# Optimization experiments

Measured on AMD Instinct MI355X. Metric: run time of the kernel, lower is better.

The kernel has to match this reference:

```python
import jax, jax.numpy as jnp
import numpy as np

B, T, D, H = 2, 2048, 1024, 16
HD = D // H  # 64


def _rotary_tables(t, hd):
    # standard RoPE cos/sin tables, shape [T, hd]
    inv_freq = 1.0 / (10000.0 ** (jnp.arange(0, hd, 2, dtype=jnp.float32) / hd))
    freqs = jnp.arange(t, dtype=jnp.float32)[:, None] * inv_freq[None, :]  # [T, hd/2]
    emb = jnp.concatenate([freqs, freqs], axis=-1)  # [T, hd]
    return jnp.cos(emb), jnp.sin(emb)


def setup_inputs() -> dict:
    key = jax.random.key(0)
    kx, kq, kk, kv, kp = jax.random.split(key, 5)
    x = jax.random.normal(kx, (B, T, D), dtype=jnp.float32)
    cos_t, sin_t = _rotary_tables(T, HD)
    cos = jnp.broadcast_to(cos_t[None], (B, T, HD)).astype(jnp.float32)
    sin = jnp.broadcast_to(sin_t[None], (B, T, HD)).astype(jnp.float32)
    scale = 0.02
    Wq = jax.random.normal(kq, (D, D), dtype=jnp.float32) * scale
    Wk = jax.random.normal(kk, (D, D), dtype=jnp.float32) * scale
    Wv = jax.random.normal(kv, (D, D), dtype=jnp.float32) * scale
    Wp = jax.random.normal(kp, (D, D), dtype=jnp.float32) * scale
    return {"x": x, "cos": cos, "sin": sin, "Wq": Wq, "Wk": Wk, "Wv": Wv, "Wp": Wp}


def _rotate_half(x):
    x1, x2 = jnp.split(x, 2, axis=-1)
    return jnp.concatenate([-x2, x1], axis=-1)


def reference(x, cos, sin, Wq, Wk, Wv, Wp):
    b, t, d = x.shape
    h, hd = H, HD
    # torch Linear: y = x @ W.T
    q = jnp.einsum('btd,ed->bte', x, Wq).reshape(b, t, h, hd)
    k = jnp.einsum('btd,ed->bte', x, Wk).reshape(b, t, h, hd)
    v = jnp.einsum('btd,ed->bte', x, Wv).reshape(b, t, h, hd)
    # RoPE, cos/sin [B,T,hd] -> broadcast over heads (unsqueeze_dim=2)
    c = cos[:, :, None, :]
    s = sin[:, :, None, :]
    q = q * c + _rotate_half(q) * s
    k = k * c + _rotate_half(k) * s
    # causal attention, softmax scale = 1/sqrt(head_dim) (flash_attn default)
    scale = 1.0 / np.sqrt(hd).astype(np.float32)
    scores = jnp.einsum('bqhd,bkhd->bhqk', q, k) * scale  # [B,H,T,T]
    mask = jnp.tril(jnp.ones((t, t), dtype=bool))
    scores = jnp.where(mask[None, None], scores, jnp.finfo(scores.dtype).min)
    probs = jax.nn.softmax(scores, axis=-1)
    out = jnp.einsum('bhqk,bkhd->bqhd', probs, v).reshape(b, t, d)
    return jnp.einsum('btd,ed->bte', out, Wp)
```

## Files before the change

### kernel.cpp

```cpp
#include <hip/hip_runtime.h>
#include <hip/hip_bf16.h>

typedef __attribute__((ext_vector_type(8))) short bf16x8s;
typedef __attribute__((ext_vector_type(4))) float f32x4;
typedef __attribute__((ext_vector_type(16))) float f32x16;
typedef __attribute__((ext_vector_type(4))) __bf16 bf16x4;
typedef __attribute__((ext_vector_type(8))) __bf16 bf16x8;

typedef const __attribute__((address_space(1))) void gvoid_t;
typedef __attribute__((address_space(3))) void lvoid_t;

constexpr int Bc = 2, Tc = 2048, Dc = 1024, Hc = 16, HDc = 64;
constexpr int Mc = Bc * Tc;

__global__ void cvt_all(const float* __restrict__ x,
                        const float* __restrict__ wq, const float* __restrict__ wk,
                        const float* __restrict__ wv, const float* __restrict__ wp,
                        __bf16* __restrict__ xb, __bf16* __restrict__ wb) {
  const int bid = blockIdx.x;
  const float* src;
  __bf16* dst;
  int i;
  if (bid < 4096) {
    src = x; dst = xb; i = (bid * 256 + threadIdx.x) * 4;
  } else {
    const int r = bid - 4096;
    const int w = r >> 10;
    src = (w == 0) ? wq : (w == 1) ? wk : (w == 2) ? wv : wp;
    dst = wb + (size_t)w * (Dc * Dc);
    i = ((r & 1023) * 256 + threadIdx.x) * 4;
  }
  float4 v = *(const float4*)(src + i);
  bf16x4 o;
  o[0] = (__bf16)v.x; o[1] = (__bf16)v.y; o[2] = (__bf16)v.z; o[3] = (__bf16)v.w;
  *(bf16x4*)(dst + i) = o;
}

__launch_bounds__(256, 2)
__global__ void gemm_qkv(const __bf16* __restrict__ A,
                         const __bf16* __restrict__ W,
                         __bf16* __restrict__ outb,
                         __bf16* __restrict__ vtout,
                         const float* __restrict__ cbt,
                         const float* __restrict__ sbt) {
  __shared__ __bf16 smem[2][128 * 64];
  __bf16* Alds = smem[0];
  __bf16* Blds = smem[1];
  const int tid = threadIdx.x;
  const int lane = tid & 63, wid = tid >> 6;
  const int wr = wid >> 1, wc = wid & 1;
  const int lr = lane & 15, lg = lane >> 4;
  const int lid = blockIdx.x + (int)gridDim.x * blockIdx.y;
  const int xcd = lid & 7, g = lid >> 3;
  const int brow = (xcd * 4 + (g & 3)) * 128;
  const int bcol = (g >> 2) * 128;
  const __bf16* Wm = W + (size_t)blockIdx.z * (Dc * Dc);

  f32x4 acc[4][4] = {};

  const char* Ag = (const char*)(A + (size_t)brow * Dc);
  const char* Bg = (const char*)(Wm + (size_t)bcol * Dc);
  const int r0 = tid >> 3;
  const int cb = (tid & 7) * 16;

  for (int k0 = 0; k0 < Dc; k0 += 64) {
#pragma unroll
    for (int i = 0; i < 4; ++i) {
      const int r = i * 32 + r0;
      const int ldsoff = (i * 256 + wid * 64) * 16;
      __builtin_amdgcn_global_load_lds(
          (gvoid_t*)(Ag + (size_t)r * (Dc * 2) + k0 * 2 + cb),
          (lvoid_t*)((char*)Alds + ldsoff), 16, 0, 0);
      __builtin_amdgcn_global_load_lds(
          (gvoid_t*)(Bg + (size_t)r * (Dc * 2) + k0 * 2 + cb),
          (lvoid_t*)((char*)Blds + ldsoff), 16, 0, 0);
    }
    __syncthreads();
#pragma unroll
    for (int kk = 0; kk < 2; ++kk) {
      const int col = kk * 32 + lg * 8;
      bf16x8s af[4], bfv[4];
#pragma unroll
      for (int m = 0; m < 4; ++m)
        af[m] = *(const bf16x8s*)(Alds + (wr * 64 + m * 16 + lr) * 64 + col);
#pragma unroll
      for (int n = 0; n < 4; ++n)
        bfv[n] = *(const bf16x8s*)(Blds + (wc * 64 + n * 16 + lr) * 64 + col);
#pragma unroll
      for (int m = 0; m < 4; ++m)
#pragma unroll
        for (int n = 0; n < 4; ++n)
          acc[m][n] = __builtin_amdgcn_mfma_f32_16x16x32_bf16(af[m], bfv[n], acc[m][n], 0, 0, 0);
    }
    __syncthreads();
  }

  const int z = blockIdx.z;
  if (z == 2) {
    const int bb = brow >> 11, t0b = brow & (Tc - 1);
    __bf16* tile_t = smem[0];
#pragma unroll
    for (int h2 = 0; h2 < 2; ++h2) {
      __syncthreads();
      if (wc == h2) {
#pragma unroll
        for (int n = 0; n < 4; ++n) {
#pragma unroll
          for (int m = 0; m < 4; ++m) {
            bf16x4 pb;
#pragma unroll
            for (int j = 0; j < 4; ++j) pb[j] = (__bf16)acc[m][n][j];
            *(bf16x4*)(tile_t + (n * 16 + lr) * 136 + wr * 64 + m * 16 + lg * 4) = pb;
          }
        }
      }
      __syncthreads();
#pragma unroll
      for (int pass = 0; pass < 4; ++pass) {
        const int r = pass * 16 + (tid >> 4);
        const int c8 = (tid & 15) * 8;
        bf16x8 vvv = *(const bf16x8*)(tile_t + r * 136 + c8);
        const int gn = bcol + h2 * 64 + r;
        const int h = gn >> 6, hd = gn & 63;
        *(bf16x8*)(vtout + (((size_t)bb * Hc + h) * HDc + hd) * Tc + t0b + c8) = vvv;
      }
    }
    return;
  }

  {
    const float scl = (z == 0) ? 0.18033688011112042f : 1.0f;
#pragma unroll
    for (int m = 0; m < 4; ++m) {
#pragma unroll
      for (int j = 0; j < 4; ++j) {
        const int gm = brow + wr * 64 + m * 16 + lg * 4 + j;
        const float* cbase = cbt + (size_t)gm * HDc;
        const float* sbase = sbt + (size_t)gm * HDc;
#pragma unroll
        for (int n = 0; n < 2; ++n) {
          const int i = n * 16 + lr;
          const float c0 = cbase[i], s0 = sbase[i];
          const float v0 = acc[m][n][j], v1 = acc[m][n + 2][j];
          acc[m][n][j]     = (v0 * c0 - v1 * s0) * scl;
          acc[m][n + 2][j] = (v1 * c0 + v0 * s0) * scl;
        }
      }
    }
    __bf16* dst = outb + (size_t)z * ((size_t)Mc * Dc);
#pragma unroll
    for (int m = 0; m < 4; ++m) {
#pragma unroll
      for (int j = 0; j < 4; ++j) {
        const int gm = brow + wr * 64 + m * 16 + lg * 4 + j;
        const int bb = gm >> 11, t = gm & (Tc - 1);
#pragma unroll
        for (int n = 0; n < 4; ++n) {
          const int gn = bcol + wc * 64 + n * 16 + lr;
          const int h = gn >> 6, hd = gn & 63;
          dst[(((size_t)bb * Hc + h) * Tc + t) * HDc + hd] = (__bf16)acc[m][n][j];
        }
      }
    }
  }
}

__launch_bounds__(256, 2)
__global__ void gemm_proj(const __bf16* __restrict__ A, const __bf16* __restrict__ W,
                          float* __restrict__ outf) {
  __shared__ __bf16 Alds[128 * 64];
  __shared__ __bf16 Blds[64 * 64];
  const int tid = threadIdx.x;
  const int lane = tid & 63, wid = tid >> 6;
  const int lr = lane & 15, lg = lane >> 4;
  const int lid = blockIdx.x + (int)gridDim.x * blockIdx.y;
  const int xcd = lid & 7, g = lid >> 3;
  const int brow = (xcd * 4 + (g & 3)) * 128;
  const int bcol = (g >> 2) * 64;
  f32x4 acc[2][4] = {};
  const char* Ag = (const char*)(A + (size_t)brow * Dc);
  const char* Bg = (const char*)(W + (size_t)bcol * Dc);
  const int r0 = tid >> 3;
  const int cb = (tid & 7) * 16;
  for (int k0 = 0; k0 < Dc; k0 += 64) {
#pragma unroll
    for (int i = 0; i < 4; ++i) {
      const int r = i * 32 + r0;
      const int ldsoff = (i * 256 + wid * 64) * 16;
      __builtin_amdgcn_global_load_lds(
          (gvoid_t*)(Ag + (size_t)r * (Dc * 2) + k0 * 2 + cb),
          (lvoid_t*)((char*)Alds + ldsoff), 16, 0, 0);
    }
#pragma unroll
    for (int i = 0; i < 2; ++i) {
      const int r = i * 32 + r0;
      const int ldsoff = (i * 256 + wid * 64) * 16;
      __builtin_amdgcn_global_load_lds(
          (gvoid_t*)(Bg + (size_t)r * (Dc * 2) + k0 * 2 + cb),
          (lvoid_t*)((char*)Blds + ldsoff), 16, 0, 0);
    }
    __syncthreads();
#pragma unroll
    for (int kk = 0; kk < 2; ++kk) {
      const int col = kk * 32 + lg * 8;
      bf16x8s af[2], bfv[4];
#pragma unroll
      for (int m = 0; m < 2; ++m)
        af[m] = *(const bf16x8s*)(Alds + (wid * 32 + m * 16 + lr) * 64 + col);
#pragma unroll
      for (int n = 0; n < 4; ++n)
        bfv[n] = *(const bf16x8s*)(Blds + (n * 16 + lr) * 64 + col);
#pragma unroll
      for (int m = 0; m < 2; ++m)
#pragma unroll
        for (int n = 0; n < 4; ++n)
          acc[m][n] = __builtin_amdgcn_mfma_f32_16x16x32_bf16(bfv[n], af[m], acc[m][n], 0, 0, 0);
    }
    __syncthreads();
  }
#pragma unroll
  for (int m = 0; m < 2; ++m) {
    const int gm = brow + wid * 32 + m * 16 + lr;
    float* rowp = outf + (size_t)gm * Dc + bcol;
#pragma unroll
    for (int n = 0; n < 4; ++n) {
      float4 fv;
      fv.x = acc[m][n][0]; fv.y = acc[m][n][1]; fv.z = acc[m][n][2]; fv.w = acc[m][n][3];
      *(float4*)(rowp + n * 16 + lg * 4) = fv;
    }
  }
}

__launch_bounds__(512, 4)
__global__ void attn_kernel(const __bf16* __restrict__ Q, const __bf16* __restrict__ K,
                            const __bf16* __restrict__ Vt, __bf16* __restrict__ O) {
  __shared__ __bf16 Klds[2][128 * 64];
  __shared__ __bf16 Vlds[2][64 * 128];
  const int f = blockIdx.x;
  const int xcd = f & 7, g = f >> 3;
  const int pass = g >> 4, g4 = g & 15;
  const int bh = xcd * 4 + pass;
  const int qt = ((pass >> 1) & 1) ? (15 - g4) : g4;
  const int tid = threadIdx.x;
  const int lane = tid & 63, wid = tid >> 6;
  const int qq = wid >> 1, kp = wid & 1;
  const int q31 = lane & 31, hh = lane >> 5;
  const int k3 = q31 & 7;
  const int v15 = q31 & 15;
  const __bf16* Qp = Q + (size_t)bh * Tc * HDc;
  const char* Kb = (const char*)(K + (size_t)bh * Tc * HDc);
  const char* Vb = (const char*)(Vt + (size_t)bh * HDc * Tc);

  const int units = qt + 1;

  const int sr = tid >> 3;
  const int sxor = ((tid & 7) ^ (sr & 7)) << 4;
  const int vr = tid >> 4;
  const int vxor = ((tid & 15) ^ (vr & 15)) << 4;
  const char* vsrc = Vb + (size_t)vr * (Tc * 2) + vxor;

  const int q0w = qt * 128 + qq * 32;
  bf16x8s qf[4];
#pragma unroll
  for (int ks = 0; ks < 4; ++ks)
    qf[ks] = *(const bf16x8s*)(Qp + (q0w + q31) * HDc + ks * 16 + hh * 8);

  const int b = bh >> 4, h = bh & 15;

  f32x16 acc0 = {}, acc1 = {};
  float lsum = 0.f;

#define STAGE(IT, BUF)                                                                   \
  do {                                                                                   \
    _Pragma("unroll")                                                                    \
    for (int i_ = 0; i_ < 2; ++i_) {                                                     \
      __builtin_amdgcn_global_load_lds(                                                  \
          (gvoid_t*)(Kb + (size_t)((IT) * 128 + i_ * 64 + sr) * 128 + sxor),             \
          (lvoid_t*)((char*)Klds[BUF] + i_ * 8192 + wid * 1024), 16, 0, 0);              \
      __builtin_amdgcn_global_load_lds(                                                  \
          (gvoid_t*)(vsrc + (size_t)i_ * 32 * (Tc * 2) + (IT) * 256),                    \
          (lvoid_t*)((char*)Vlds[BUF] + i_ * 8192 + wid * 1024), 16, 0, 0);              \
    }                                                                                    \
  } while (0)

  STAGE(0, 0);
  asm volatile("s_waitcnt vmcnt(0)" ::: "memory");
  __builtin_amdgcn_sched_barrier(0);
  __builtin_amdgcn_s_barrier();
  __builtin_amdgcn_sched_barrier(0);

  for (int u = 0; u < units; ++u) {
    if (u + 1 < units) STAGE(u + 1, (u + 1) & 1);
    __builtin_amdgcn_sched_barrier(0);

    const bool last = (u == qt);
    if (!(last && kp == 1 && qq < 2)) {
      const char* Kl = (const char*)Klds[u & 1];
      const char* Vl = (const char*)Vlds[u & 1];
      const bool fin = last && ((qq >> 1) == kp);
      const int thr = q0w + q31 - u * 128 - kp * 64 - 4 * hh;

#pragma unroll
      for (int ct = 0; ct < 2; ++ct) {
        bf16x8s kf[4];
#pragma unroll
        for (int ks = 0; ks < 4; ++ks)
          kf[ks] = *(const bf16x8s*)(Kl + (kp * 64 + ct * 32 + q31) * 128 +
                                     (((2 * ks + hh) ^ k3) << 4));
        f32x16 z = {};
        __builtin_amdgcn_s_setprio(1);
#pragma unroll
        for (int ks = 0; ks < 4; ++ks)
          z = __builtin_amdgcn_mfma_f32_32x32x16_bf16(kf[ks], qf[ks], z, 0, 0, 0);
        __builtin_amdgcn_s_setprio(0);

        unsigned w0[4], w1[4];
#pragma unroll
        for (int n = 0; n < 4; ++n) {
          float e[4];
#pragma unroll
          for (int j = 0; j < 4; ++j) {
            float ev = __builtin_amdgcn_exp2f(z[n * 4 + j]);
            if (fin && (ct * 32 + n * 8 + j > thr)) ev = 0.f;
            lsum += ev;
            e[j] = ev;
          }
          asm("v_cvt_pk_bf16_f32 %0, %1, %2" : "=v"(w0[n]) : "v"(e[0]), "v"(e[1]));
          asm("v_cvt_pk_bf16_f32 %0, %1, %2" : "=v"(w1[n]) : "v"(e[2]), "v"(e[3]));
        }

        bf16x8s pfr[2];
#pragma unroll
        for (int ks2 = 0; ks2 < 2; ++ks2) {
          unsigned a = w0[2 * ks2], bb2 = w0[2 * ks2 + 1];
          unsigned c = w1[2 * ks2], d = w1[2 * ks2 + 1];
          asm volatile("v_permlane32_swap_b32 %0, %1" : "+v"(a), "+v"(bb2));
          asm volatile("v_permlane32_swap_b32 %0, %1" : "+v"(c), "+v"(d));
          union { unsigned u[4]; bf16x8s v; } uu;
          uu.u[0] = a; uu.u[1] = c; uu.u[2] = bb2; uu.u[3] = d;
          pfr[ks2] = uu.v;
        }

        __builtin_amdgcn_s_setprio(1);
#pragma unroll
        for (int ks2 = 0; ks2 < 2; ++ks2) {
          const int so = ((kp * 8 + ct * 4 + 2 * ks2 + hh) ^ v15) << 4;
          const bf16x8s va0 = *(const bf16x8s*)(Vl + q31 * 256 + so);
          const bf16x8s va1 = *(const bf16x8s*)(Vl + (32 + q31) * 256 + so);
          acc0 = __builtin_amdgcn_mfma_f32_32x32x16_bf16(va0, pfr[ks2], acc0, 0, 0, 0);
          acc1 = __builtin_amdgcn_mfma_f32_32x32x16_bf16(va1, pfr[ks2], acc1, 0, 0, 0);
        }
        __builtin_amdgcn_s_setprio(0);
      }
    }

    if (u + 1 < units) {
      asm volatile("s_waitcnt vmcnt(0)" ::: "memory");
      __builtin_amdgcn_sched_barrier(0);
      __builtin_amdgcn_s_barrier();
      __builtin_amdgcn_sched_barrier(0);
    }
  }
#undef STAGE

  __syncthreads();
  float* kscr = (float*)&Klds[0][0];
  float* lscr = (float*)&Vlds[0][0];
  if (kp == 1) {
#pragma unroll
    for (int i = 0; i < 16; ++i) {
      kscr[qq * 2048 + i * 64 + lane] = acc0[i];
      kscr[qq * 2048 + 1024 + i * 64 + lane] = acc1[i];
    }
    lscr[qq * 64 + lane] = lsum;
  }
  __syncthreads();
  if (kp == 0) {
#pragma unroll
    for (int i = 0; i < 16; ++i) {
      acc0[i] += kscr[qq * 2048 + i * 64 + lane];
      acc1[i] += kscr[qq * 2048 + 1024 + i * 64 + lane];
    }
    lsum += lscr[qq * 64 + lane];
    const float lt = lsum + __shfl_xor(lsum, 32);
    const float linv = 1.f / lt;
    const int t = q0w + q31;
    __bf16* dst = O + ((size_t)b * Tc + t) * Dc + h * HDc;
#pragma unroll
    for (int qd = 0; qd < 4; ++qd) {
      bf16x4 o0, o1;
#pragma unroll
      for (int j = 0; j < 4; ++j) {
        o0[j] = (__bf16)(acc0[qd * 4 + j] * linv);
        o1[j] = (__bf16)(acc1[qd * 4 + j] * linv);
      }
      *(bf16x4*)(dst + qd * 8 + hh * 4) = o0;
      *(bf16x4*)(dst + 32 + qd * 8 + hh * 4) = o1;
    }
  }
}

extern "C" void kernel_launch(void* const* d_in, const int* in_sizes, int n_in,
                              void* d_out, int out_size, void* d_ws, size_t ws_size,
                              hipStream_t stream) {
  const float* x   = (const float*)d_in[0];
  const float* cbt = (const float*)d_in[1];
  const float* sbt = (const float*)d_in[2];
  const float* Wq  = (const float*)d_in[3];
  const float* Wk  = (const float*)d_in[4];
  const float* Wv  = (const float*)d_in[5];
  const float* Wp  = (const float*)d_in[6];
  float* out = (float*)d_out;
  char* ws = (char*)d_ws;
  __bf16* xb = (__bf16*)(ws);
  __bf16* wb = (__bf16*)(ws + (8u << 20));
  __bf16* qb = (__bf16*)(ws + (16u << 20));
  __bf16* vt = (__bf16*)(ws + (40u << 20));
  __bf16* ao = (__bf16*)(ws + (48u << 20));
  __bf16* kb = qb + (size_t)Mc * Dc;

  cvt_all<<<8192, 256, 0, stream>>>(x, Wq, Wk, Wv, Wp, xb, wb);
  gemm_qkv<<<dim3(8, 32, 3), 256, 0, stream>>>(xb, wb, qb, vt, cbt, sbt);
  attn_kernel<<<512, 512, 0, stream>>>(qb, kb, vt, ao);
  gemm_proj<<<dim3(16, 32), 256, 0, stream>>>(ao, wb + 3u * (Dc * Dc), out);
}
```

Measured before the change: 95.30 us.

## Fuse Q/K/V GEMMs into one block with double-buffered swizzled LDS

The QKV projection kernel now computes the Q, K and V output tiles for the same 128-row A tile in a single 512-thread block. Each A tile is staged once instead of three times. Global-to-LDS loads are double-buffered so the next K-slice is fetched while MFMAs run on the current one. LDS columns are XOR-swizzled to reduce bank conflicts, and MFMA sections raise wave priority. The cost is a large LDS footprint of about 128KB, which limits the kernel to one block per CU. The grid also shrinks to 256 blocks, which removes the z-dimension parallelism.

```diff
diff --git a/kernel.cpp b/kernel.cpp
--- a/kernel.cpp
+++ b/kernel.cpp
@@ -36,130 +36,142 @@
   *(bf16x4*)(dst + i) = o;
 }
 
-__launch_bounds__(256, 2)
+__launch_bounds__(512, 2)
 __global__ void gemm_qkv(const __bf16* __restrict__ A,
                          const __bf16* __restrict__ W,
                          __bf16* __restrict__ outb,
                          __bf16* __restrict__ vtout,
                          const float* __restrict__ cbt,
                          const float* __restrict__ sbt) {
-  __shared__ __bf16 smem[2][128 * 64];
-  __bf16* Alds = smem[0];
-  __bf16* Blds = smem[1];
+  __shared__ __bf16 Albuf[2][128 * 64];
+  __shared__ __bf16 Bbuf[2][3][128 * 64];
   const int tid = threadIdx.x;
   const int lane = tid & 63, wid = tid >> 6;
   const int wr = wid >> 1, wc = wid & 1;
   const int lr = lane & 15, lg = lane >> 4;
-  const int lid = blockIdx.x + (int)gridDim.x * blockIdx.y;
+  const int lid = blockIdx.x + 8 * blockIdx.y;
   const int xcd = lid & 7, g = lid >> 3;
   const int brow = (xcd * 4 + (g & 3)) * 128;
   const int bcol = (g >> 2) * 128;
-  const __bf16* Wm = W + (size_t)blockIdx.z * (Dc * Dc);
-
-  f32x4 acc[4][4] = {};
+
+  f32x4 acc[3][2][4] = {};
 
   const char* Ag = (const char*)(A + (size_t)brow * Dc);
-  const char* Bg = (const char*)(Wm + (size_t)bcol * Dc);
-  const int r0 = tid >> 3;
-  const int cb = (tid & 7) * 16;
-
-  for (int k0 = 0; k0 < Dc; k0 += 64) {
-#pragma unroll
-    for (int i = 0; i < 4; ++i) {
-      const int r = i * 32 + r0;
-      const int ldsoff = (i * 256 + wid * 64) * 16;
-      __builtin_amdgcn_global_load_lds(
-          (gvoid_t*)(Ag + (size_t)r * (Dc * 2) + k0 * 2 + cb),
-          (lvoid_t*)((char*)Alds + ldsoff), 16, 0, 0);
-      __builtin_amdgcn_global_load_lds(
-          (gvoid_t*)(Bg + (size_t)r * (Dc * 2) + k0 * 2 + cb),
-          (lvoid_t*)((char*)Blds + ldsoff), 16, 0, 0);
-    }
-    __syncthreads();
+  const char* Bg = (const char*)(W + (size_t)bcol * Dc);
+  const int r0s = tid >> 3;
+  const int scol = (((tid & 7) ^ (r0s & 7)) << 4);
+  const int lr7 = lr & 7;
+
+#define STAGE(K0, BUF)                                                                    \
+  do {                                                                                    \
+    _Pragma("unroll")                                                                     \
+    for (int i_ = 0; i_ < 2; ++i_) {                                                      \
+      __builtin_amdgcn_global_load_lds(                                                   \
+          (gvoid_t*)(Ag + (size_t)(i_ * 64 + r0s) * (Dc * 2) + (K0)*2 + scol),            \
+          (lvoid_t*)((char*)Albuf[BUF] + i_ * 8192 + wid * 1024), 16, 0, 0);              \
+      _Pragma("unroll")                                                                   \
+      for (int z_ = 0; z_ < 3; ++z_)                                                      \
+        __builtin_amdgcn_global_load_lds(                                                 \
+            (gvoid_t*)(Bg + (size_t)z_ * (Dc * Dc * 2) +                                  \
+                       (size_t)(i_ * 64 + r0s) * (Dc * 2) + (K0)*2 + scol),               \
+            (lvoid_t*)((char*)Bbuf[BUF][z_] + i_ * 8192 + wid * 1024), 16, 0, 0);         \
+    }                                                                                     \
+  } while (0)
+
+  STAGE(0, 0);
+  asm volatile("s_waitcnt vmcnt(0)" ::: "memory");
+  __builtin_amdgcn_sched_barrier(0);
+  __builtin_amdgcn_s_barrier();
+  __builtin_amdgcn_sched_barrier(0);
+
+  for (int s = 0; s < 16; ++s) {
+    if (s + 1 < 16) STAGE((s + 1) * 64, (s + 1) & 1);
+    __builtin_amdgcn_sched_barrier(0);
+    const char* Al = (const char*)Albuf[s & 1];
+    const char* Bl0 = (const char*)Bbuf[s & 1][0];
 #pragma unroll
     for (int kk = 0; kk < 2; ++kk) {
-      const int col = kk * 32 + lg * 8;
-      bf16x8s af[4], bfv[4];
-#pragma unroll
-      for (int m = 0; m < 4; ++m)
-        af[m] = *(const bf16x8s*)(Alds + (wr * 64 + m * 16 + lr) * 64 + col);
-#pragma unroll
-      for (int n = 0; n < 4; ++n)
-        bfv[n] = *(const bf16x8s*)(Blds + (wc * 64 + n * 16 + lr) * 64 + col);
-#pragma unroll
-      for (int m = 0; m < 4; ++m)
+      const int sw = ((kk * 4 + lg) ^ lr7) << 4;
+      bf16x8s af[2];
+#pragma unroll
+      for (int m = 0; m < 2; ++m)
+        af[m] = *(const bf16x8s*)(Al + (wr * 32 + m * 16 + lr) * 128 + sw);
+#pragma unroll
+      for (int z = 0; z < 3; ++z) {
+        const char* Bl = Bl0 + z * (128 * 64 * 2);
+        bf16x8s bfv[4];
 #pragma unroll
         for (int n = 0; n < 4; ++n)
-          acc[m][n] = __builtin_amdgcn_mfma_f32_16x16x32_bf16(af[m], bfv[n], acc[m][n], 0, 0, 0);
-    }
-    __syncthreads();
-  }
-
-  const int z = blockIdx.z;
-  if (z == 2) {
-    const int bb = brow >> 11, t0b = brow & (Tc - 1);
-    __bf16* tile_t = smem[0];
+          bfv[n] = *(const bf16x8s*)(Bl + (wc * 64 + n * 16 + lr) * 128 + sw);
+        __builtin_amdgcn_s_setprio(1);
+#pragma unroll
+        for (int m = 0; m < 2; ++m)
+#pragma unroll
+          for (int n = 0; n < 4; ++n)
+            acc[z][m][n] =
+                __builtin_amdgcn_mfma_f32_16x16x32_bf16(af[m], bfv[n], acc[z][m][n], 0, 0, 0);
+        __builtin_amdgcn_s_setprio(0);
+      }
+    }
+    asm volatile("s_waitcnt vmcnt(0)" ::: "memory");
+    __builtin_amdgcn_sched_barrier(0);
+    __builtin_amdgcn_s_barrier();
+    __builtin_amdgcn_sched_barrier(0);
+  }
+#undef STAGE
+
+  const int h = (bcol >> 6) + wc;
+#pragma unroll
+  for (int z = 0; z < 2; ++z) {
+    const float scl = (z == 0) ? 0.18033688011112042f : 1.0f;
+    __bf16* dst = outb + (size_t)z * ((size_t)Mc * Dc);
+#pragma unroll
+    for (int m = 0; m < 2; ++m) {
+#pragma unroll
+      for (int j = 0; j < 4; ++j) {
+        const int gm = brow + wr * 32 + m * 16 + lg * 4 + j;
+        const int bb = gm >> 11, t = gm & (Tc - 1);
+        const float* cbase = cbt + (size_t)gm * HDc;
+        const float* sbase = sbt + (size_t)gm * HDc;
+#pragma unroll
+        for (int n = 0; n < 2; ++n) {
+          const int i = n * 16 + lr;
+          const float c0 = cbase[i], s0 = sbase[i];
+          const float v0 = acc[z][m][n][j], v1 = acc[z][m][n + 2][j];
+          acc[z][m][n][j]     = (v0 * c0 - v1 * s0) * scl;
+          acc[z][m][n + 2][j] = (v1 * c0 + v0 * s0) * scl;
+        }
+        __bf16* rowp = dst + (((size_t)bb * Hc + h) * Tc + t) * HDc;
+#pragma unroll
+        for (int n = 0; n < 4; ++n) rowp[n * 16 + lr] = (__bf16)acc[z][m][n][j];
+      }
+    }
+  }
+
+  {
+    const int bb2 = brow >> 11, t0b = brow & (Tc - 1);
+    __bf16* tile_t = (__bf16*)Albuf;
 #pragma unroll
     for (int h2 = 0; h2 < 2; ++h2) {
       __syncthreads();
       if (wc == h2) {
 #pragma unroll
-        for (int n = 0; n < 4; ++n) {
-#pragma unroll
-          for (int m = 0; m < 4; ++m) {
-            bf16x4 pb;
-#pragma unroll
-            for (int j = 0; j < 4; ++j) pb[j] = (__bf16)acc[m][n][j];
-            *(bf16x4*)(tile_t + (n * 16 + lr) * 136 + wr * 64 + m * 16 + lg * 4) = pb;
-          }
-        }
+        for (int n = 0; n < 4; ++n)
+#pragma unroll
+          for (int m = 0; m < 2; ++m)
+#pragma unroll
+            for (int j = 0; j < 4; ++j)
+              tile_t[(n * 16 + lr) * 136 + wr * 32 + m * 16 + lg * 4 + j] =
+                  (__bf16)acc[2][m][n][j];
       }
       __syncthreads();
-#pragma unroll
-      for (int pass = 0; pass < 4; ++pass) {
-        const int r = pass * 16 + (tid >> 4);
+      const int hh2 = (bcol >> 6) + h2;
+#pragma unroll
+      for (int p = 0; p < 2; ++p) {
+        const int r = p * 32 + (tid >> 4);
         const int c8 = (tid & 15) * 8;
         bf16x8 vvv = *(const bf16x8*)(tile_t + r * 136 + c8);
-        const int gn = bcol + h2 * 64 + r;
-        const int h = gn >> 6, hd = gn & 63;
-        *(bf16x8*)(vtout + (((size_t)bb * Hc + h) * HDc + hd) * Tc + t0b + c8) = vvv;
-      }
-    }
-    return;
-  }
-
-  {
-    const float scl = (z == 0) ? 0.18033688011112042f : 1.0f;
-#pragma unroll
-    for (int m = 0; m < 4; ++m) {
-#pragma unroll
-      for (int j = 0; j < 4; ++j) {
-        const int gm = brow + wr * 64 + m * 16 + lg * 4 + j;
-        const float* cbase = cbt + (size_t)gm * HDc;
-        const float* sbase = sbt + (size_t)gm * HDc;
-#pragma unroll
-        for (int n = 0; n < 2; ++n) {
-          const int i = n * 16 + lr;
-          const float c0 = cbase[i], s0 = sbase[i];
-          const float v0 = acc[m][n][j], v1 = acc[m][n + 2][j];
-          acc[m][n][j]     = (v0 * c0 - v1 * s0) * scl;
-          acc[m][n + 2][j] = (v1 * c0 + v0 * s0) * scl;
-        }
-      }
-    }
-    __bf16* dst = outb + (size_t)z * ((size_t)Mc * Dc);
-#pragma unroll
-    for (int m = 0; m < 4; ++m) {
-#pragma unroll
-      for (int j = 0; j < 4; ++j) {
-        const int gm = brow + wr * 64 + m * 16 + lg * 4 + j;
-        const int bb = gm >> 11, t = gm & (Tc - 1);
-#pragma unroll
-        for (int n = 0; n < 4; ++n) {
-          const int gn = bcol + wc * 64 + n * 16 + lr;
-          const int h = gn >> 6, hd = gn & 63;
-          dst[(((size_t)bb * Hc + h) * Tc + t) * HDc + hd] = (__bf16)acc[m][n][j];
-        }
+        *(bf16x8*)(vtout + (((size_t)bb2 * Hc + hh2) * HDc + r) * Tc + t0b + c8) = vvv;
       }
     }
   }
@@ -420,7 +432,7 @@
   __bf16* kb = qb + (size_t)Mc * Dc;
 
   cvt_all<<<8192, 256, 0, stream>>>(x, Wq, Wk, Wv, Wp, xb, wb);
-  gemm_qkv<<<dim3(8, 32, 3), 256, 0, stream>>>(xb, wb, qb, vt, cbt, sbt);
+  gemm_qkv<<<dim3(8, 32), 512, 0, stream>>>(xb, wb, qb, vt, cbt, sbt);
   attn_kernel<<<512, 512, 0, stream>>>(qb, kb, vt, ao);
   gemm_proj<<<dim3(16, 32), 256, 0, stream>>>(ao, wb + 3u * (Dc * Dc), out);
 }
```

Result: no change. 95.52 us (+0.2%).
